# Kernel optimization log

Measured on AMD Instinct MI355X. Metric: run time of the kernel, lower is better.

## Reference

```python
import jax, jax.numpy as jnp
import numpy as np

B, S, D, F, E = 8, 4096, 512, 2048, 8
INIT_LAMBDA = 0.2
LN_EPS = 1e-5
LN_MERGE = 0.03  # scale used when merging layer_norm expert task-vectors


def setup_inputs() -> dict:
    key = jax.random.key(0)
    ks = jax.random.split(key, 12)
    n = lambda k, shp, s=1.0: jax.random.normal(k, shp, dtype=jnp.float32) * s
    return {
        "hidden_states": n(ks[0], (B, S, D)),
        # DictMoEGate (2 hidden layers): fc1 ~ N(0, 0.01), fc2 bias = init_lambda
        "gfc1_w": n(ks[1], (D, D), 0.01),
        "gfc1_b": jnp.zeros((D,), jnp.float32),
        "gfc2_w": n(ks[2], (E, D), 0.01),
        "gfc2_b": jnp.full((E,), INIT_LAMBDA, dtype=jnp.float32),
        # base PositionWiseFeedForward params (torch Linear layout: [out, in])
        "W1": n(ks[3], (F, D), 0.02),
        "b1": jnp.zeros((F,), jnp.float32),
        "W2": n(ks[4], (D, F), 0.02),
        "b2": jnp.zeros((D,), jnp.float32),
        "ln_g": jnp.ones((D,), jnp.float32),
        "ln_b": jnp.zeros((D,), jnp.float32),
        # expert task vectors (expert_sd - base_sd), one per base param
        "tv_W1": n(ks[5], (E, F, D), 0.02),
        "tv_b1": n(ks[6], (E, F), 0.02),
        "tv_W2": n(ks[7], (E, D, F), 0.02),
        "tv_b2": n(ks[8], (E, D), 0.02),
        "tv_ln_g": n(ks[9], (E, D), 0.02),
        "tv_ln_b": n(ks[10], (E, D), 0.02),
    }


def reference(hidden_states, gfc1_w, gfc1_b, gfc2_w, gfc2_b,
              W1, b1, W2, b2, ln_g, ln_b,
              tv_W1, tv_b1, tv_W2, tv_b2, tv_ln_g, tv_ln_b):
    x = hidden_states  # [B, S, D] (batch_first)
    # --- gate: per-token 2-layer MLP, then mean over sequence -> [B, E] ---
    gh = jax.nn.relu(jnp.einsum('bsd,hd->bsh', x, gfc1_w) + gfc1_b)
    g = (jnp.einsum('bsh,eh->bse', gh, gfc2_w) + gfc2_b).mean(axis=1)  # [B, E]
    # --- per-sample merged weights: base + sum_e g[b,e] * task_vector[e] ---
    W1m = W1 + jnp.einsum('be,efd->bfd', g, tv_W1)   # [B, F, D]
    b1m = b1 + g @ tv_b1                              # [B, F]
    W2m = W2 + jnp.einsum('be,edf->bdf', g, tv_W2)   # [B, D, F]
    b2m = b2 + g @ tv_b2                              # [B, D]
    # layer_norm params: sd = param + sum_e (tv_e - param) * 0.03 (gate-independent)
    lng = ln_g + LN_MERGE * (tv_ln_g - ln_g).sum(axis=0)  # [D]
    lnb = ln_b + LN_MERGE * (tv_ln_b - ln_b).sum(axis=0)  # [D]
    # --- PositionWiseFeedForward with per-sample weights (dropout = eval/identity) ---
    h = jax.nn.relu(jnp.einsum('bsd,bfd->bsf', x, W1m) + b1m[:, None, :])  # [B, S, F]
    out = jnp.einsum('bsf,bdf->bsd', h, W2m) + b2m[:, None, :]             # [B, S, D]
    res = x + out
    mu = res.mean(axis=-1, keepdims=True)
    var = res.var(axis=-1, keepdims=True)
    return (res - mu) * jax.lax.rsqrt(var + LN_EPS) * lng + lnb
```

## Files before the change

### kernel.cpp

```cpp
#include <hip/hip_runtime.h>

typedef __bf16 bf16;
typedef __attribute__((ext_vector_type(8))) __bf16 bf16x8;
typedef __attribute__((ext_vector_type(4))) float f32x4;

#define LDS16(gp, lp)                                                          \
  __builtin_amdgcn_global_load_lds(                                            \
      (const __attribute__((address_space(1))) void*)(gp),                     \
      (__attribute__((address_space(3))) void*)(lp), 16, 0, 0)

__global__ __launch_bounds__(256) void cast_bf16_kernel(const float* __restrict__ src,
                                                        bf16* __restrict__ dst, int n) {
  int i = (blockIdx.x * 256 + threadIdx.x) * 8;
  if (i < n) {
    float4 a = *(const float4*)(src + i);
    float4 b = *(const float4*)(src + i + 4);
    bf16x8 v;
    v[0] = (bf16)a.x; v[1] = (bf16)a.y; v[2] = (bf16)a.z; v[3] = (bf16)a.w;
    v[4] = (bf16)b.x; v[5] = (bf16)b.y; v[6] = (bf16)b.z; v[7] = (bf16)b.w;
    *(bf16x8*)(dst + i) = v;
  }
}

__global__ __launch_bounds__(256) void zero_kernel(float* p, int n) {
  int i = blockIdx.x * 256 + threadIdx.x;
  if (i < n) p[i] = 0.f;
}

template <int MODE, int KTILES>
__global__ __launch_bounds__(256) void gemm_bt(const bf16* __restrict__ A,
                                               const bf16* __restrict__ B0, long bstride,
                                               const float* __restrict__ bias, long biasStride,
                                               const float* __restrict__ resid,
                                               float* __restrict__ fout,
                                               bf16* __restrict__ hout) {
  constexpr int K = KTILES * 64;
  __shared__ bf16 smem[2 * 128 * 64];
  bf16* As = smem;
  bf16* Bs = smem + 8192;
  const int tid = threadIdx.x;
  const int lane = tid & 63, wv = tid >> 6;
  const int wm = wv >> 1, wn = wv & 1;
  const int lr = lane & 15, q = lane >> 4;
  const int b = blockIdx.z;
  const long blockM = (long)b * 4096 + (long)blockIdx.x * 128;
  const int blockN = blockIdx.y * 128;
  const bf16* Bp = B0 + (long)b * bstride;

  f32x4 acc[4][4] = {};

  const bf16* Ab = A + blockM * K;
  const bf16* Bb = Bp + (long)blockN * K;
  const int srow = lane >> 3;
  const int scol = ((lane & 7) ^ srow) * 8;

  for (int it = 0; it < KTILES; ++it) {
    const int k0 = it * 64;
#pragma unroll
    for (int c = 0; c < 4; ++c) {
      int n = wv * 4 + c;
      int row = n * 8 + srow;
      LDS16(Ab + (long)row * K + k0 + scol, &As[n * 512]);
      LDS16(Bb + (long)row * K + k0 + scol, &Bs[n * 512]);
    }
    __syncthreads();
#pragma unroll
    for (int ks = 0; ks < 2; ++ks) {
      const int c0 = ks * 4 + q;
      const int sw = lane & 7;
      bf16x8 af[4], bfr[4];
#pragma unroll
      for (int i = 0; i < 4; ++i)
        af[i] = *(const bf16x8*)&As[(wm * 64 + i * 16 + lr) * 64 + ((c0 ^ sw) * 8)];
#pragma unroll
      for (int j = 0; j < 4; ++j)
        bfr[j] = *(const bf16x8*)&Bs[(wn * 64 + j * 16 + lr) * 64 + ((c0 ^ sw) * 8)];
#pragma unroll
      for (int i = 0; i < 4; ++i)
#pragma unroll
        for (int j = 0; j < 4; ++j)
          acc[i][j] = __builtin_amdgcn_mfma_f32_16x16x32_bf16(af[i], bfr[j], acc[i][j], 0, 0, 0);
    }
    __syncthreads();
  }

  if (MODE == 0) {
#pragma unroll
    for (int j = 0; j < 4; ++j) {
      const int gc = blockN + wn * 64 + j * 16 + lr;
      const float bv = bias[gc];
      float s = 0.f;
#pragma unroll
      for (int i = 0; i < 4; ++i)
#pragma unroll
        for (int r = 0; r < 4; ++r) {
          float v = acc[i][j][r] + bv;
          s += v > 0.f ? v : 0.f;
        }
      s += __shfl_xor(s, 16);
      s += __shfl_xor(s, 32);
      if (q == 0) atomicAdd(&fout[b * 512 + gc], s);
    }
  } else if (MODE == 1) {
#pragma unroll
    for (int j = 0; j < 4; ++j) {
      const int gc = wn * 64 + j * 16 + lr;
      const float bv = bias[(long)b * biasStride + blockN + gc];
#pragma unroll
      for (int i = 0; i < 4; ++i)
#pragma unroll
        for (int r = 0; r < 4; ++r) {
          const int lrow = wm * 64 + i * 16 + q * 4 + r;
          float v = acc[i][j][r] + bv;
          smem[lrow * 128 + gc] = (bf16)(v > 0.f ? v : 0.f);
        }
    }
    __syncthreads();
#pragma unroll
    for (int p = 0; p < 8; ++p) {
      const int row = p * 16 + (tid >> 4);
      const int col = (tid & 15) * 8;
      *(bf16x8*)&hout[(blockM + row) * 2048 + blockN + col] =
          *(const bf16x8*)&smem[row * 128 + col];
    }
  } else {
#pragma unroll
    for (int j = 0; j < 4; ++j) {
      const int gc = blockN + wn * 64 + j * 16 + lr;
      const float bv = bias[(long)b * biasStride + gc];
#pragma unroll
      for (int i = 0; i < 4; ++i)
#pragma unroll
        for (int r = 0; r < 4; ++r) {
          const long gr = blockM + wm * 64 + i * 16 + q * 4 + r;
          fout[gr * 512 + gc] = acc[i][j][r] + bv + resid[gr * 512 + gc];
        }
    }
  }
}

__global__ __launch_bounds__(512) void small_kernel(
    const float* __restrict__ ghsum, const float* __restrict__ g2w,
    const float* __restrict__ g2b, const float* __restrict__ lngI,
    const float* __restrict__ lnbI, const float* __restrict__ tvlg,
    const float* __restrict__ tvlb, const float* __restrict__ b1,
    const float* __restrict__ tvb1, const float* __restrict__ b2,
    const float* __restrict__ tvb2, float* __restrict__ g, float* __restrict__ lng,
    float* __restrict__ lnb, float* __restrict__ b1m, float* __restrict__ b2m) {
  __shared__ float gs[64];
  const int t = threadIdx.x;
  if (t < 64) {
    const int b = t >> 3, e = t & 7;
    float s = 0.f;
    for (int h = 0; h < 512; ++h) s += ghsum[b * 512 + h] * g2w[e * 512 + h];
    float gv = s * (1.f / 4096.f) + g2b[e];
    gs[t] = gv;
    g[t] = gv;
  }
  __syncthreads();
  if (t < 512) {
    float lg = lngI[t], lb = lnbI[t], sg = 0.f, sb = 0.f;
    for (int e = 0; e < 8; ++e) { sg += tvlg[e * 512 + t]; sb += tvlb[e * 512 + t]; }
    lng[t] = lg + 0.03f * (sg - 8.f * lg);
    lnb[t] = lb + 0.03f * (sb - 8.f * lb);
  }
  for (int i = t; i < 8 * 2048; i += 512) {
    const int b = i >> 11, f = i & 2047;
    float s = b1[f];
    for (int e = 0; e < 8; ++e) s += gs[b * 8 + e] * tvb1[e * 2048 + f];
    b1m[i] = s;
  }
  for (int i = t; i < 8 * 512; i += 512) {
    const int b = i >> 9, d = i & 511;
    float s = b2[d];
    for (int e = 0; e < 8; ++e) s += gs[b * 8 + e] * tvb2[e * 512 + d];
    b2m[i] = s;
  }
}

__global__ __launch_bounds__(256) void merge_kernel(
    const float* __restrict__ W1, const float* __restrict__ tvW1,
    const float* __restrict__ W2, const float* __restrict__ tvW2,
    const float* __restrict__ g, bf16* __restrict__ W1m, bf16* __restrict__ W2m) {
  int idx = blockIdx.x * 256 + threadIdx.x;
  if (idx < 1048576) {
    const float w = W1[idx];
    float tv[8];
#pragma unroll
    for (int e = 0; e < 8; ++e) tv[e] = tvW1[(long)e * 1048576 + idx];
#pragma unroll
    for (int b = 0; b < 8; ++b) {
      float s = w;
#pragma unroll
      for (int e = 0; e < 8; ++e) s += g[b * 8 + e] * tv[e];
      W1m[(long)b * 1048576 + idx] = (bf16)s;
    }
  } else {
    idx -= 1048576;
    const float w = W2[idx];
    float tv[8];
#pragma unroll
    for (int e = 0; e < 8; ++e) tv[e] = tvW2[(long)e * 1048576 + idx];
#pragma unroll
    for (int b = 0; b < 8; ++b) {
      float s = w;
#pragma unroll
      for (int e = 0; e < 8; ++e) s += g[b * 8 + e] * tv[e];
      W2m[(long)b * 1048576 + idx] = (bf16)s;
    }
  }
}

__global__ __launch_bounds__(256) void ln_kernel(float* __restrict__ out,
                                                 const float* __restrict__ lng,
                                                 const float* __restrict__ lnb) {
  const int wv = threadIdx.x >> 6, lane = threadIdx.x & 63;
  const long row = (long)blockIdx.x * 4 + wv;
  float* p = out + row * 512 + lane * 8;
  float4 a = *(float4*)p;
  float4 b = *(float4*)(p + 4);
  float v[8] = {a.x, a.y, a.z, a.w, b.x, b.y, b.z, b.w};
  float s1 = 0.f, s2 = 0.f;
#pragma unroll
  for (int k = 0; k < 8; ++k) { s1 += v[k]; s2 += v[k] * v[k]; }
#pragma unroll
  for (int off = 32; off > 0; off >>= 1) {
    s1 += __shfl_xor(s1, off);
    s2 += __shfl_xor(s2, off);
  }
  const float mean = s1 * (1.f / 512.f);
  const float var = s2 * (1.f / 512.f) - mean * mean;
  const float rstd = rsqrtf(var + 1e-5f);
  const int c = lane * 8;
  float o[8];
#pragma unroll
  for (int k = 0; k < 8; ++k) o[k] = (v[k] - mean) * rstd * lng[c + k] + lnb[c + k];
  *(float4*)p = make_float4(o[0], o[1], o[2], o[3]);
  *(float4*)(p + 4) = make_float4(o[4], o[5], o[6], o[7]);
}

extern "C" void kernel_launch(void* const* d_in, const int* in_sizes, int n_in,
                              void* d_out, int out_size, void* d_ws, size_t ws_size,
                              hipStream_t stream) {
  const float* x    = (const float*)d_in[0];
  const float* g1w  = (const float*)d_in[1];
  const float* g1b  = (const float*)d_in[2];
  const float* g2w  = (const float*)d_in[3];
  const float* g2b  = (const float*)d_in[4];
  const float* W1   = (const float*)d_in[5];
  const float* b1   = (const float*)d_in[6];
  const float* W2   = (const float*)d_in[7];
  const float* b2   = (const float*)d_in[8];
  const float* lngI = (const float*)d_in[9];
  const float* lnbI = (const float*)d_in[10];
  const float* tvW1 = (const float*)d_in[11];
  const float* tvb1 = (const float*)d_in[12];
  const float* tvW2 = (const float*)d_in[13];
  const float* tvb2 = (const float*)d_in[14];
  const float* tvlg = (const float*)d_in[15];
  const float* tvlb = (const float*)d_in[16];
  float* out = (float*)d_out;

  char* w = (char*)d_ws;
  bf16*  x_bf   = (bf16*)(w);
  bf16*  g1w_bf = (bf16*)(w + 33554432);
  bf16*  W1m    = (bf16*)(w + 34078720);
  bf16*  W2m    = (bf16*)(w + 50855936);
  bf16*  h      = (bf16*)(w + 67633152);
  float* ghsum  = (float*)(w + 201850880);
  float* g      = (float*)(w + 201867264);
  float* b1m    = (float*)(w + 201867520);
  float* b2m    = (float*)(w + 201933056);
  float* lng    = (float*)(w + 201949440);
  float* lnb    = (float*)(w + 201951488);

  cast_bf16_kernel<<<8192, 256, 0, stream>>>(x, x_bf, 16777216);
  cast_bf16_kernel<<<128, 256, 0, stream>>>(g1w, g1w_bf, 262144);
  zero_kernel<<<16, 256, 0, stream>>>(ghsum, 4096);
  gemm_bt<0, 8><<<dim3(32, 4, 8), 256, 0, stream>>>(x_bf, g1w_bf, 0, g1b, 0,
                                                    nullptr, ghsum, nullptr);
  small_kernel<<<1, 512, 0, stream>>>(ghsum, g2w, g2b, lngI, lnbI, tvlg, tvlb,
                                      b1, tvb1, b2, tvb2, g, lng, lnb, b1m, b2m);
  merge_kernel<<<8192, 256, 0, stream>>>(W1, tvW1, W2, tvW2, g, W1m, W2m);
  gemm_bt<1, 8><<<dim3(32, 16, 8), 256, 0, stream>>>(x_bf, W1m, 1048576, b1m, 2048,
                                                     nullptr, nullptr, h);
  gemm_bt<2, 32><<<dim3(32, 4, 8), 256, 0, stream>>>(h, W2m, 1048576, b2m, 512,
                                                     x, out, nullptr);
  ln_kernel<<<8192, 256, 0, stream>>>(out, lng, lnb);
}
```

Before: 483.6 us.

## Fuse second FFN GEMM with residual and LayerNorm; vectorize weight merge

Replaces the second GEMM plus separate LayerNorm pass with one kernel in which each 512-thread block computes a full 128x512 output row tile. It adds bias and the residual, reduces row statistics across waves through LDS, and writes normalized output directly. This removes the fp32 intermediate round-trip through global memory and one launch. The merge kernel also now processes four elements per thread with float4 loads and bf16x4 stores. The cost is a grid of only 256 blocks and A fragments loaded straight from global memory without LDS staging, which may reduce occupancy and latency hiding in the largest GEMM.

```diff
diff --git a/kernel.cpp b/kernel.cpp
--- a/kernel.cpp
+++ b/kernel.cpp
@@ -1,6 +1,7 @@
 #include <hip/hip_runtime.h>
 
 typedef __bf16 bf16;
+typedef __attribute__((ext_vector_type(4))) __bf16 bf16x4;
 typedef __attribute__((ext_vector_type(8))) __bf16 bf16x8;
 typedef __attribute__((ext_vector_type(4))) float f32x4;
 
@@ -31,7 +32,6 @@
 __global__ __launch_bounds__(256) void gemm_bt(const bf16* __restrict__ A,
                                                const bf16* __restrict__ B0, long bstride,
                                                const float* __restrict__ bias, long biasStride,
-                                               const float* __restrict__ resid,
                                                float* __restrict__ fout,
                                                bf16* __restrict__ hout) {
   constexpr int K = KTILES * 64;
@@ -101,7 +101,7 @@
       s += __shfl_xor(s, 32);
       if (q == 0) atomicAdd(&fout[b * 512 + gc], s);
     }
-  } else if (MODE == 1) {
+  } else {
 #pragma unroll
     for (int j = 0; j < 4; ++j) {
       const int gc = wn * 64 + j * 16 + lr;
@@ -123,20 +123,117 @@
       *(bf16x8*)&hout[(blockM + row) * 2048 + blockN + col] =
           *(const bf16x8*)&smem[row * 128 + col];
     }
-  } else {
-#pragma unroll
-    for (int j = 0; j < 4; ++j) {
-      const int gc = blockN + wn * 64 + j * 16 + lr;
-      const float bv = bias[(long)b * biasStride + gc];
-#pragma unroll
-      for (int i = 0; i < 4; ++i)
-#pragma unroll
-        for (int r = 0; r < 4; ++r) {
-          const long gr = blockM + wm * 64 + i * 16 + q * 4 + r;
-          fout[gr * 512 + gc] = acc[i][j][r] + bv + resid[gr * 512 + gc];
-        }
-    }
-  }
+  }
+}
+
+__global__ __launch_bounds__(512) void ffn2_ln_kernel(
+    const bf16* __restrict__ h, const bf16* __restrict__ W2m,
+    const float* __restrict__ b2m, const float* __restrict__ xres,
+    const float* __restrict__ lng, const float* __restrict__ lnb,
+    float* __restrict__ out) {
+  __shared__ bf16 Bs[512 * 64];
+  const int tid = threadIdx.x;
+  const int lane = tid & 63, wv = tid >> 6;
+  const int wm = wv >> 2, wn = wv & 3;
+  const int lr = lane & 15, q = lane >> 4;
+  const int b = blockIdx.z;
+  const long blockM = (long)b * 4096 + (long)blockIdx.x * 128;
+  const bf16* Bb = W2m + (long)b * 1048576;
+  const bf16* Ab = h + blockM * 2048;
+
+  f32x4 acc[4][8] = {};
+  const int srow = lane >> 3;
+  const int scol = ((lane & 7) ^ srow) * 8;
+
+  for (int it = 0; it < 32; ++it) {
+    const int k0 = it * 64;
+    bf16x8 af[4][2];
+#pragma unroll
+    for (int i = 0; i < 4; ++i)
+#pragma unroll
+      for (int kk = 0; kk < 2; ++kk)
+        af[i][kk] = *(const bf16x8*)(Ab + (long)(wm * 64 + i * 16 + lr) * 2048 +
+                                     k0 + kk * 32 + q * 8);
+#pragma unroll
+    for (int c = 0; c < 8; ++c) {
+      int grp = wv * 8 + c;
+      int row = grp * 8 + srow;
+      LDS16(Bb + (long)row * 2048 + k0 + scol, &Bs[grp * 512]);
+    }
+    __syncthreads();
+#pragma unroll
+    for (int kk = 0; kk < 2; ++kk) {
+      bf16x8 bfr[8];
+#pragma unroll
+      for (int j = 0; j < 8; ++j) {
+        int n = wn * 128 + j * 16 + lr;
+        bfr[j] = *(const bf16x8*)&Bs[n * 64 + (((kk * 4 + q) ^ (n & 7)) * 8)];
+      }
+#pragma unroll
+      for (int i = 0; i < 4; ++i)
+#pragma unroll
+        for (int j = 0; j < 8; ++j)
+          acc[i][j] = __builtin_amdgcn_mfma_f32_16x16x32_bf16(af[i][kk], bfr[j], acc[i][j], 0, 0, 0);
+    }
+    __syncthreads();
+  }
+
+  float bv[8], lg[8], lb[8];
+  int gc[8];
+#pragma unroll
+  for (int j = 0; j < 8; ++j) {
+    gc[j] = wn * 128 + j * 16 + lr;
+    bv[j] = b2m[b * 512 + gc[j]];
+    lg[j] = lng[gc[j]];
+    lb[j] = lnb[gc[j]];
+  }
+  float p1[4][4], p2[4][4];
+#pragma unroll
+  for (int i = 0; i < 4; ++i)
+#pragma unroll
+    for (int r = 0; r < 4; ++r) {
+      const long gr = blockM + wm * 64 + i * 16 + q * 4 + r;
+      float s1 = 0.f, s2 = 0.f;
+#pragma unroll
+      for (int j = 0; j < 8; ++j) {
+        float v = acc[i][j][r] + bv[j] + xres[gr * 512 + gc[j]];
+        acc[i][j][r] = v;
+        s1 += v;
+        s2 += v * v;
+      }
+      s1 += __shfl_xor(s1, 1); s2 += __shfl_xor(s2, 1);
+      s1 += __shfl_xor(s1, 2); s2 += __shfl_xor(s2, 2);
+      s1 += __shfl_xor(s1, 4); s2 += __shfl_xor(s2, 4);
+      s1 += __shfl_xor(s1, 8); s2 += __shfl_xor(s2, 8);
+      p1[i][r] = s1;
+      p2[i][r] = s2;
+    }
+  float2* P = (float2*)Bs;
+  if (lr == 0) {
+#pragma unroll
+    for (int i = 0; i < 4; ++i)
+#pragma unroll
+      for (int r = 0; r < 4; ++r)
+        P[(wm * 64 + i * 16 + q * 4 + r) * 4 + wn] = make_float2(p1[i][r], p2[i][r]);
+  }
+  __syncthreads();
+#pragma unroll
+  for (int i = 0; i < 4; ++i)
+#pragma unroll
+    for (int r = 0; r < 4; ++r) {
+      const int row = wm * 64 + i * 16 + q * 4 + r;
+      float2 a0 = P[row * 4 + 0], a1 = P[row * 4 + 1];
+      float2 a2 = P[row * 4 + 2], a3 = P[row * 4 + 3];
+      const float s1 = a0.x + a1.x + a2.x + a3.x;
+      const float s2 = a0.y + a1.y + a2.y + a3.y;
+      const float mean = s1 * (1.f / 512.f);
+      const float var = s2 * (1.f / 512.f) - mean * mean;
+      const float rstd = rsqrtf(var + 1e-5f);
+      const long gr = blockM + row;
+#pragma unroll
+      for (int j = 0; j < 8; ++j)
+        out[gr * 512 + gc[j]] = (acc[i][j][r] - mean) * rstd * lg[j] + lb[j];
+    }
 }
 
 __global__ __launch_bounds__(512) void small_kernel(
@@ -182,61 +279,33 @@
     const float* __restrict__ W1, const float* __restrict__ tvW1,
     const float* __restrict__ W2, const float* __restrict__ tvW2,
     const float* __restrict__ g, bf16* __restrict__ W1m, bf16* __restrict__ W2m) {
-  int idx = blockIdx.x * 256 + threadIdx.x;
+  int idx = (blockIdx.x * 256 + threadIdx.x) * 4;
+  const float* Wp;
+  const float* tvp;
+  bf16* outp;
   if (idx < 1048576) {
-    const float w = W1[idx];
-    float tv[8];
-#pragma unroll
-    for (int e = 0; e < 8; ++e) tv[e] = tvW1[(long)e * 1048576 + idx];
-#pragma unroll
-    for (int b = 0; b < 8; ++b) {
-      float s = w;
-#pragma unroll
-      for (int e = 0; e < 8; ++e) s += g[b * 8 + e] * tv[e];
-      W1m[(long)b * 1048576 + idx] = (bf16)s;
-    }
+    Wp = W1; tvp = tvW1; outp = W1m;
   } else {
     idx -= 1048576;
-    const float w = W2[idx];
-    float tv[8];
-#pragma unroll
-    for (int e = 0; e < 8; ++e) tv[e] = tvW2[(long)e * 1048576 + idx];
-#pragma unroll
-    for (int b = 0; b < 8; ++b) {
-      float s = w;
-#pragma unroll
-      for (int e = 0; e < 8; ++e) s += g[b * 8 + e] * tv[e];
-      W2m[(long)b * 1048576 + idx] = (bf16)s;
-    }
-  }
-}
-
-__global__ __launch_bounds__(256) void ln_kernel(float* __restrict__ out,
-                                                 const float* __restrict__ lng,
-                                                 const float* __restrict__ lnb) {
-  const int wv = threadIdx.x >> 6, lane = threadIdx.x & 63;
-  const long row = (long)blockIdx.x * 4 + wv;
-  float* p = out + row * 512 + lane * 8;
-  float4 a = *(float4*)p;
-  float4 b = *(float4*)(p + 4);
-  float v[8] = {a.x, a.y, a.z, a.w, b.x, b.y, b.z, b.w};
-  float s1 = 0.f, s2 = 0.f;
-#pragma unroll
-  for (int k = 0; k < 8; ++k) { s1 += v[k]; s2 += v[k] * v[k]; }
-#pragma unroll
-  for (int off = 32; off > 0; off >>= 1) {
-    s1 += __shfl_xor(s1, off);
-    s2 += __shfl_xor(s2, off);
-  }
-  const float mean = s1 * (1.f / 512.f);
-  const float var = s2 * (1.f / 512.f) - mean * mean;
-  const float rstd = rsqrtf(var + 1e-5f);
-  const int c = lane * 8;
-  float o[8];
-#pragma unroll
-  for (int k = 0; k < 8; ++k) o[k] = (v[k] - mean) * rstd * lng[c + k] + lnb[c + k];
-  *(float4*)p = make_float4(o[0], o[1], o[2], o[3]);
-  *(float4*)(p + 4) = make_float4(o[4], o[5], o[6], o[7]);
+    Wp = W2; tvp = tvW2; outp = W2m;
+  }
+  float4 w = *(const float4*)(Wp + idx);
+  float4 tv[8];
+#pragma unroll
+  for (int e = 0; e < 8; ++e) tv[e] = *(const float4*)(tvp + (long)e * 1048576 + idx);
+#pragma unroll
+  for (int b = 0; b < 8; ++b) {
+    float4 s = w;
+#pragma unroll
+    for (int e = 0; e < 8; ++e) {
+      const float ge = g[b * 8 + e];
+      s.x += ge * tv[e].x; s.y += ge * tv[e].y;
+      s.z += ge * tv[e].z; s.w += ge * tv[e].w;
+    }
+    bf16x4 o;
+    o[0] = (bf16)s.x; o[1] = (bf16)s.y; o[2] = (bf16)s.z; o[3] = (bf16)s.w;
+    *(bf16x4*)(outp + (long)b * 1048576 + idx) = o;
+  }
 }
 
 extern "C" void kernel_launch(void* const* d_in, const int* in_sizes, int n_in,
@@ -278,13 +347,11 @@
   cast_bf16_kernel<<<128, 256, 0, stream>>>(g1w, g1w_bf, 262144);
   zero_kernel<<<16, 256, 0, stream>>>(ghsum, 4096);
   gemm_bt<0, 8><<<dim3(32, 4, 8), 256, 0, stream>>>(x_bf, g1w_bf, 0, g1b, 0,
-                                                    nullptr, ghsum, nullptr);
+                                                    ghsum, nullptr);
   small_kernel<<<1, 512, 0, stream>>>(ghsum, g2w, g2b, lngI, lnbI, tvlg, tvlb,
                                       b1, tvb1, b2, tvb2, g, lng, lnb, b1m, b2m);
-  merge_kernel<<<8192, 256, 0, stream>>>(W1, tvW1, W2, tvW2, g, W1m, W2m);
+  merge_kernel<<<2048, 256, 0, stream>>>(W1, tvW1, W2, tvW2, g, W1m, W2m);
   gemm_bt<1, 8><<<dim3(32, 16, 8), 256, 0, stream>>>(x_bf, W1m, 1048576, b1m, 2048,
-                                                     nullptr, nullptr, h);
-  gemm_bt<2, 32><<<dim3(32, 4, 8), 256, 0, stream>>>(h, W2m, 1048576, b2m, 512,
-                                                     x, out, nullptr);
-  ln_kernel<<<8192, 256, 0, stream>>>(out, lng, lnb);
-}
+                                                     nullptr, h);
+  ffn2_ln_kernel<<<dim3(32, 1, 8), 512, 0, stream>>>(h, W2m, b2m, x, lng, lnb, out);
+}
```

Measured after the change: 510.5 us. +5.6%, slower.
